# Optimization experiments

Hardware: AMD Instinct MI355X
Metric: run time of the kernel (lower is better)

The kernel has to match this reference:

```python
import jax, jax.numpy as jnp
import numpy as np

B, S, D = 2, 2048, 2048
H, HD = 16, 128          # num_heads, head_dim (H*HD == D)
I = 4096                 # intermediate_size; ffn in-dim is 2*I
EPS = 1e-5


def rmsnorm(x, w):
    return x * jax.lax.rsqrt(jnp.mean(x * x, axis=-1, keepdims=True) + EPS) * w


def setup_inputs() -> dict:
    key = jax.random.key(0)
    ks = jax.random.split(key, 12)
    sd = 0.02
    return {
        "hidden_states": jax.random.normal(ks[0], (B, S, D), jnp.float32),
        "attention_mask": jnp.zeros((B, S), jnp.float32),  # additive mask
        "rn1_w": jnp.ones((D,), jnp.float32),
        "wq": jax.random.normal(ks[1], (D, D), jnp.float32) * sd,
        "wk": jax.random.normal(ks[2], (D, D), jnp.float32) * sd,
        "wv": jax.random.normal(ks[3], (D, D), jnp.float32) * sd,
        "wo": jax.random.normal(ks[4], (D, D), jnp.float32) * sd,
        "rn2_w": jnp.ones((D,), jnp.float32),
        "w1": jax.random.normal(ks[5], (D, 2 * I), jnp.float32) * sd,      # Linear(d, 2*I, bias=False)
        "fc1_w": jax.random.normal(ks[6], (2 * I, I), jnp.float32) * sd,   # SwiGLU fc1
        "fc1_b": jnp.zeros((I,), jnp.float32),
        "fc2_w": jax.random.normal(ks[7], (2 * I, I), jnp.float32) * sd,   # SwiGLU fc2
        "fc2_b": jnp.zeros((I,), jnp.float32),
        "w3": jax.random.normal(ks[8], (I, D), jnp.float32) * sd,          # Linear(I, d, bias=False)
    }


def reference(hidden_states, attention_mask, rn1_w, wq, wk, wv, wo, rn2_w,
              w1, fc1_w, fc1_b, fc2_w, fc2_b, w3):
    # --- attention ---
    attn_in = rmsnorm(hidden_states, rn1_w)
    q = (attn_in @ wq).reshape(B, S, H, HD)
    k = (attn_in @ wk).reshape(B, S, H, HD)
    v = (attn_in @ wv).reshape(B, S, H, HD)
    # rope_cache is None -> no rotary embedding applied
    scores = jnp.einsum("bqhd,bkhd->bhqk", q, k) / np.sqrt(HD).astype(np.float32)
    scores = scores + attention_mask[:, None, None, :]  # [B,1,1,S] broadcast
    probs = jax.nn.softmax(scores, axis=-1)             # dropout p=0 (eval)
    attn = jnp.einsum("bhqk,bkhd->bqhd", probs, v).reshape(B, S, D)
    residual1 = hidden_states + attn @ wo
    # --- SwiGLU FFN ---
    ffn_in = rmsnorm(residual1, rn2_w)
    x = ffn_in @ w1                                      # [B,S,2I]
    gated = jax.nn.silu(x @ fc1_w + fc1_b) * (x @ fc2_w + fc2_b)  # [B,S,I]
    return residual1 + gated @ w3
```

## Files before the change

kernel.cpp:

```cpp
#include <hip/hip_runtime.h>
#include <hip/hip_bf16.h>
#include <stdint.h>

using short8 = __attribute__((ext_vector_type(8))) short;
using uint4v = __attribute__((ext_vector_type(4))) unsigned int;
using f32x4  = __attribute__((ext_vector_type(4))) float;

#define DEV __device__ __forceinline__

DEV float b2f(unsigned short u) {
  union { unsigned int i; float f; } v; v.i = ((unsigned int)u) << 16; return v.f;
}
DEV unsigned short f2b(float f) {
  union { float f; unsigned int i; } v; v.f = f;
  unsigned int x = v.i;
  return (unsigned short)((x + 0x7FFFu + ((x >> 16) & 1u)) >> 16);
}
DEV void g2lds16(const void* g, void* l) {
  __builtin_amdgcn_global_load_lds((const __attribute__((address_space(1))) void*)g,
                                   (__attribute__((address_space(3))) void*)l, 16, 0, 0);
}

DEV void xcd_rect_map(int wg, int nbx, int rby, int rbx, int& by, int& bx) {
  const int xcd_cols = nbx / rbx;
  const int xcd = wg & 7, local = wg >> 3;
  const int xr = xcd / xcd_cols, xc = xcd % xcd_cols;
  by = xr * rby + local / rbx;
  bx = xc * rbx + local % rbx;
}

enum { EPI_BF16 = 0, EPI_RESID_F32 = 1, EPI_BIAS_BF16 = 2, EPI_RESID_OUT = 3, EPI_SWIGLU = 4 };

template<int EPI>
__global__ __launch_bounds__(512, 2)
void gemm_bt256(const unsigned short* __restrict__ A, const unsigned short* __restrict__ Bt,
                void* __restrict__ Cout, const void* __restrict__ extra,
                const void* __restrict__ extra2, int M, int N, int K, int rby, int rbx) {
  __shared__ __align__(16) unsigned short As[2][256 * 64];
  __shared__ __align__(16) unsigned short Bs3[3][256 * 64];
  int by, bx;
  xcd_rect_map(blockIdx.x, N >> 8, rby, rbx, by, bx);
  const int m0 = by << 8, n0 = bx << 8;
  const int t = threadIdx.x;
  const int l = t & 63, wid = t >> 6;
  const int lr = l & 15, lg = l >> 4;
  const int wr = (wid >> 2) << 7;
  const int wc = (wid & 3) << 6;

  f32x4 acc[8][4];
#pragma unroll
  for (int i = 0; i < 8; ++i)
#pragma unroll
    for (int j = 0; j < 4; ++j) acc[i][j] = (f32x4){0.f, 0.f, 0.f, 0.f};

  const int sr = t >> 3;
  const int scSwz = ((t & 7) << 3) ^ ((sr & 7) << 3);
  const unsigned short* Ag = A  + (size_t)(m0 + sr) * K + scSwz;
  const unsigned short* Bg = Bt + (size_t)(n0 + sr) * K + scSwz;
  const int nT = K >> 6;

  const unsigned short* AgNext = Ag + 64;
  const unsigned short* BgNext2 = Bg + 128;
  const size_t rowK64 = (size_t)64 * K;

  const int xorv = (lr & 7) << 3;
  const int cb0 = (lg * 8) ^ xorv;
  const int cb1 = (32 + lg * 8) ^ xorv;

  short8 afA[2][2], afB[2][2], bfrA[4][2], bfrB[4][2];

#define STAGE_A(buf)                                                  \
  {                                                                   \
    unsigned short* dst = &As[buf][t * 8];                            \
    _Pragma("unroll")                                                 \
    for (int ld = 0; ld < 4; ++ld)                                    \
      g2lds16(AgNext + (size_t)ld * rowK64, dst + ld * 4096);         \
  }
#define STAGE_B2(slot)                                                \
  {                                                                   \
    unsigned short* dst = &Bs3[slot][t * 8];                          \
    _Pragma("unroll")                                                 \
    for (int ld = 0; ld < 4; ++ld)                                    \
      g2lds16(BgNext2 + (size_t)ld * rowK64, dst + ld * 4096);        \
  }
#define READ_A(dst, base, p)                                          \
  {                                                                   \
    const int ro0 = (wr + ((p) * 2 + 0) * 16 + lr) << 6;              \
    const int ro1 = (wr + ((p) * 2 + 1) * 16 + lr) << 6;              \
    dst[0][0] = *(const short8*)((base) + ro0 + cb0);                 \
    dst[0][1] = *(const short8*)((base) + ro0 + cb1);                 \
    dst[1][0] = *(const short8*)((base) + ro1 + cb0);                 \
    dst[1][1] = *(const short8*)((base) + ro1 + cb1);                 \
  }
#define READ_B(dst, base)                                             \
  {                                                                   \
    _Pragma("unroll")                                                 \
    for (int ni = 0; ni < 4; ++ni) {                                  \
      const int ro = (wc + ni * 16 + lr) << 6;                        \
      dst[ni][0] = *(const short8*)((base) + ro + cb0);               \
      dst[ni][1] = *(const short8*)((base) + ro + cb1);               \
    }                                                                 \
  }
#define MFMA_PH(af, bfr, r0)                                          \
  {                                                                   \
    _Pragma("unroll")                                                 \
    for (int kk = 0; kk < 2; ++kk)                                    \
      _Pragma("unroll")                                               \
      for (int a = 0; a < 2; ++a)                                     \
        _Pragma("unroll")                                             \
        for (int ni = 0; ni < 4; ++ni)                                \
          acc[(r0) + a][ni] = __builtin_amdgcn_mfma_f32_16x16x32_bf16(\
              af[a][kk], bfr[ni][kk], acc[(r0) + a][ni], 0, 0, 0);    \
  }

#define TILE_BODY(tt, BFR, BFRN)                                      \
  {                                                                   \
    const unsigned short* baseA = &As[(tt) & 1][0];                   \
    const bool more1 = ((tt) + 1) < nT;                               \
    const bool more2 = ((tt) + 2) < nT;                               \
               \
    READ_A(afB, baseA, 1);                                            \
    if (more1) STAGE_A(((tt) + 1) & 1);                               \
    asm volatile("s_waitcnt lgkmcnt(4)" ::: "memory");                \
    __builtin_amdgcn_sched_barrier(0);                                \
    __builtin_amdgcn_s_setprio(1);                                    \
    MFMA_PH(afA, BFR, 0);                                             \
    __builtin_amdgcn_s_setprio(0);                                    \
               \
    READ_A(afA, baseA, 2);                                            \
    if (more2) STAGE_B2(bs2);                                         \
    asm volatile("s_waitcnt lgkmcnt(4)" ::: "memory");                \
    __builtin_amdgcn_sched_barrier(0);                                \
    __builtin_amdgcn_s_setprio(1);                                    \
    MFMA_PH(afB, BFR, 2);                                             \
    __builtin_amdgcn_s_setprio(0);                                    \
       \
    READ_A(afB, baseA, 3);                                            \
    if (more1) {                                                      \
      if (more2) asm volatile("s_waitcnt vmcnt(8)" ::: "memory");     \
      else       asm volatile("s_waitcnt vmcnt(4)" ::: "memory");     \
    }                                                                 \
    asm volatile("s_waitcnt lgkmcnt(4)" ::: "memory");                \
    __builtin_amdgcn_sched_barrier(0);                                \
    __builtin_amdgcn_s_setprio(1);                                    \
    MFMA_PH(afA, BFR, 4);                                             \
    __builtin_amdgcn_s_setprio(0);                                    \
                 \
    if (more1) {                                                      \
      READ_B(BFRN, &Bs3[bnext][0]);                                   \
      asm volatile("s_waitcnt lgkmcnt(8)" ::: "memory");              \
    } else {                                                          \
      asm volatile("s_waitcnt lgkmcnt(0)" ::: "memory");              \
    }                                                                 \
    __builtin_amdgcn_sched_barrier(0);                                \
    __builtin_amdgcn_s_setprio(1);                                    \
    MFMA_PH(afB, BFR, 6);                                             \
    __builtin_amdgcn_s_setprio(0);                                    \
    if (more1) {                                                      \
      if (more2) asm volatile("s_waitcnt vmcnt(4)" ::: "memory");     \
      else       asm volatile("s_waitcnt vmcnt(0)" ::: "memory");     \
      asm volatile("s_barrier" ::: "memory");                         \
      AgNext += 64;                                                   \
      BgNext2 += 64;                                                  \
      bnext = (bnext == 2) ? 0 : bnext + 1;                           \
      bs2  = (bs2 == 2) ? 0 : bs2 + 1;                                \
      READ_A(afA, &As[((tt) + 1) & 1][0], 0);                         \
    }                                                                 \
  }

  {
    unsigned short* dstA = &As[0][t * 8];
    unsigned short* dstB = &Bs3[0][t * 8];
#pragma unroll
    for (int ld = 0; ld < 4; ++ld) {
      g2lds16(Ag + (size_t)ld * rowK64, dstA + ld * 4096);
      g2lds16(Bg + (size_t)ld * rowK64, dstB + ld * 4096);
    }
  }
  {
    unsigned short* dstB1 = &Bs3[1][t * 8];
    const unsigned short* srcB1 = Bg + 64;
#pragma unroll
    for (int ld = 0; ld < 4; ++ld) g2lds16(srcB1 + (size_t)ld * rowK64, dstB1 + ld * 4096);
  }
  asm volatile("s_waitcnt vmcnt(4)\n\ts_barrier" ::: "memory");

  int bnext = 1;
  int bs2 = 2;
  READ_A(afA, &As[0][0], 0);
  READ_B(bfrA, &Bs3[0][0]);

  for (int tp = 0; tp < nT; tp += 2) {
    TILE_BODY(tp,     bfrA, bfrB);
    TILE_BODY(tp + 1, bfrB, bfrA);
  }
#undef STAGE_A
#undef STAGE_B2
#undef READ_A
#undef READ_B
#undef MFMA_PH
#undef TILE_BODY

#pragma unroll
  for (int mi = 0; mi < 8; ++mi) {
#pragma unroll
    for (int ni = 0; ni < 4; ++ni) {
      const int col = n0 + wc + ni * 16 + lr;
#pragma unroll
      for (int j = 0; j < 4; ++j) {
        const int row = m0 + wr + mi * 16 + lg * 4 + j;
        const size_t idx = (size_t)row * N + col;
        const float v = acc[mi][ni][j];
        if constexpr (EPI == EPI_BF16) {
          ((unsigned short*)Cout)[idx] = f2b(v);
        } else if constexpr (EPI == EPI_RESID_F32) {
          ((float*)Cout)[idx] = v + ((const float*)extra)[idx];
        } else if constexpr (EPI == EPI_BIAS_BF16) {
          ((unsigned short*)Cout)[idx] = f2b(v + ((const float*)extra)[col]);
        } else if constexpr (EPI == EPI_SWIGLU) {
          const float g1v = b2f(((const unsigned short*)extra2)[idx]);
          const float v2 = v + ((const float*)extra)[col];
          ((unsigned short*)Cout)[idx] = f2b(g1v / (1.f + __expf(-g1v)) * v2);
        } else {
          ((float*)Cout)[idx] = v + ((const float*)extra)[idx];
        }
      }
    }
  }
}

template<int EPI>
__global__ __launch_bounds__(256)
void gemm_bt(const unsigned short* __restrict__ A, const unsigned short* __restrict__ Bt,
             void* __restrict__ Cout, const void* __restrict__ extra,
             int M, int N, int K, int rby, int rbx) {
  __shared__ __align__(16) unsigned short As[128 * 64];
  __shared__ __align__(16) unsigned short Bs[128 * 64];
  int by, bx;
  xcd_rect_map(blockIdx.x, N >> 7, rby, rbx, by, bx);
  const int m0 = by << 7, n0 = bx << 7;
  const int t = threadIdx.x;
  const int l = t & 63, w = t >> 6;
  const int lr = l & 15, lg = l >> 4;
  const int wr = (w >> 1) << 6, wc = (w & 1) << 6;

  f32x4 acc[4][4];
#pragma unroll
  for (int i = 0; i < 4; ++i)
#pragma unroll
    for (int j = 0; j < 4; ++j) acc[i][j] = (f32x4){0.f, 0.f, 0.f, 0.f};

  const int sr = t >> 3;
  const int skSwz = ((t & 7) << 3) ^ ((sr & 7) << 3);
  const unsigned short* Ag = A  + (size_t)(m0 + sr) * K + skSwz;
  const unsigned short* Bg = Bt + (size_t)(n0 + sr) * K + skSwz;
  unsigned short* Al = As + t * 8;
  unsigned short* Bl = Bs + t * 8;

  for (int kt = 0; kt < K; kt += 64) {
#pragma unroll
    for (int c = 0; c < 4; ++c) {
      g2lds16(Ag + (size_t)(c * 32) * K + kt, Al + c * 2048);
      g2lds16(Bg + (size_t)(c * 32) * K + kt, Bl + c * 2048);
    }
    __syncthreads();
#pragma unroll
    for (int ks = 0; ks < 2; ++ks) {
      short8 af[4], bfr[4];
#pragma unroll
      for (int mi = 0; mi < 4; ++mi) {
        const int row = wr + mi * 16 + lr;
        af[mi] = *(const short8*)(As + (row << 6) + (((ks * 32 + lg * 8)) ^ ((row & 7) << 3)));
      }
#pragma unroll
      for (int ni = 0; ni < 4; ++ni) {
        const int row = wc + ni * 16 + lr;
        bfr[ni] = *(const short8*)(Bs + (row << 6) + (((ks * 32 + lg * 8)) ^ ((row & 7) << 3)));
      }
#pragma unroll
      for (int mi = 0; mi < 4; ++mi)
#pragma unroll
        for (int ni = 0; ni < 4; ++ni)
          acc[mi][ni] = __builtin_amdgcn_mfma_f32_16x16x32_bf16(af[mi], bfr[ni], acc[mi][ni], 0, 0, 0);
    }
    __syncthreads();
  }

#pragma unroll
  for (int mi = 0; mi < 4; ++mi) {
#pragma unroll
    for (int ni = 0; ni < 4; ++ni) {
      const int col = n0 + wc + ni * 16 + lr;
#pragma unroll
      for (int j = 0; j < 4; ++j) {
        const int row = m0 + wr + mi * 16 + lg * 4 + j;
        const size_t idx = (size_t)row * N + col;
        const float v = acc[mi][ni][j];
        if constexpr (EPI == EPI_BF16) {
          ((unsigned short*)Cout)[idx] = f2b(v);
        } else if constexpr (EPI == EPI_RESID_F32) {
          ((float*)Cout)[idx] = v + ((const float*)extra)[idx];
        } else if constexpr (EPI == EPI_BIAS_BF16) {
          ((unsigned short*)Cout)[idx] = f2b(v + ((const float*)extra)[col]);
        } else {
          ((float*)Cout)[idx] = v + ((const float*)extra)[idx];
        }
      }
    }
  }
}

__global__ __launch_bounds__(256)
void attn_fwd(const unsigned short* __restrict__ qkv, const unsigned short* __restrict__ vt,
              const float* __restrict__ mask, unsigned short* __restrict__ out) {
  __shared__ __align__(16) unsigned short Ks[64 * 128];
  __shared__ __align__(16) unsigned short Vs[128 * 64];
  __shared__ __align__(16) unsigned short Ps[4][16 * 64];
  const int b = blockIdx.z, hh = blockIdx.y;
  const int q0 = blockIdx.x << 6;
  const int t = threadIdx.x, l = t & 63, w = t >> 6;
  const int lr = l & 15, lg = l >> 4;
  const float scale = 0.08838834764831845f;

  short8 qf[4];
  {
    const unsigned short* qb = qkv + (size_t)(b * 2048 + q0 + w * 16 + lr) * 6144 + hh * 128;
#pragma unroll
    for (int ks = 0; ks < 4; ++ks) qf[ks] = *(const short8*)(qb + ks * 32 + lg * 8);
  }
  f32x4 acc_o[8];
#pragma unroll
  for (int i = 0; i < 8; ++i) acc_o[i] = (f32x4){0.f, 0.f, 0.f, 0.f};
  float m_r[4], l_r[4];
#pragma unroll
  for (int j = 0; j < 4; ++j) { m_r[j] = -1e30f; l_r[j] = 0.f; }

  const unsigned short* kb = qkv + (size_t)(b * 2048) * 6144 + 2048 + hh * 128;
  const unsigned short* vb = vt + (size_t)(b * 16 + hh) * 128 * 2048;
  const float* mb = mask + b * 2048;

  for (int kt = 0; kt < 2048; kt += 64) {
#pragma unroll
    for (int c = 0; c < 4; ++c) {
      const int e = (c * 256 + t) * 8;
      const int kr = e >> 7, kc = e & 127;
      g2lds16(kb + (size_t)(kt + kr) * 6144 + (kc ^ ((kr & 7) << 3)), Ks + e);
      const int vr = e >> 6, vc = e & 63;
      g2lds16(vb + (size_t)vr * 2048 + kt + (vc ^ ((vr & 7) << 3)), Vs + e);
    }
    __syncthreads();

    f32x4 sc[4];
#pragma unroll
    for (int nt = 0; nt < 4; ++nt) {
      f32x4 s = (f32x4){0.f, 0.f, 0.f, 0.f};
#pragma unroll
      for (int ks = 0; ks < 4; ++ks) {
        short8 kf = *(const short8*)(Ks + ((nt * 16 + lr) << 7) + ((ks * 32 + lg * 8) ^ ((lr & 7) << 3)));
        s = __builtin_amdgcn_mfma_f32_16x16x32_bf16(qf[ks], kf, s, 0, 0, 0);
      }
      sc[nt] = s;
    }
#pragma unroll
    for (int nt = 0; nt < 4; ++nt) {
      const float mv = mb[kt + nt * 16 + lr];
#pragma unroll
      for (int j = 0; j < 4; ++j) sc[nt][j] = sc[nt][j] * scale + mv;
    }
#pragma unroll
    for (int j = 0; j < 4; ++j) {
      float tm = fmaxf(fmaxf(sc[0][j], sc[1][j]), fmaxf(sc[2][j], sc[3][j]));
      tm = fmaxf(tm, __shfl_xor(tm, 1));
      tm = fmaxf(tm, __shfl_xor(tm, 2));
      tm = fmaxf(tm, __shfl_xor(tm, 4));
      tm = fmaxf(tm, __shfl_xor(tm, 8));
      const float mn = fmaxf(m_r[j], tm);
      const float corr = __expf(m_r[j] - mn);
      m_r[j] = mn;
      float ps = 0.f;
#pragma unroll
      for (int nt = 0; nt < 4; ++nt) {
        const float p = __expf(sc[nt][j] - mn);
        sc[nt][j] = p;
        ps += p;
      }
      ps += __shfl_xor(ps, 1);
      ps += __shfl_xor(ps, 2);
      ps += __shfl_xor(ps, 4);
      ps += __shfl_xor(ps, 8);
      l_r[j] = l_r[j] * corr + ps;
#pragma unroll
      for (int di = 0; di < 8; ++di) acc_o[di][j] *= corr;
    }
#pragma unroll
    for (int nt = 0; nt < 4; ++nt)
#pragma unroll
      for (int j = 0; j < 4; ++j) {
        const int q = lg * 4 + j;
        Ps[w][(q << 6) + ((nt * 16 + lr) ^ ((q & 7) << 3))] = f2b(sc[nt][j]);
      }
    asm volatile("s_waitcnt lgkmcnt(0)" ::: "memory");
#pragma unroll
    for (int ks2 = 0; ks2 < 2; ++ks2) {
      short8 pf = *(const short8*)(&Ps[w][(lr << 6) + ((ks2 * 32 + lg * 8) ^ ((lr & 7) << 3))]);
#pragma unroll
      for (int di = 0; di < 8; ++di) {
        short8 vf = *(const short8*)(Vs + ((di * 16 + lr) << 6) + ((ks2 * 32 + lg * 8) ^ ((lr & 7) << 3)));
        acc_o[di] = __builtin_amdgcn_mfma_f32_16x16x32_bf16(pf, vf, acc_o[di], 0, 0, 0);
      }
    }
    __syncthreads();
  }
#pragma unroll
  for (int di = 0; di < 8; ++di)
#pragma unroll
    for (int j = 0; j < 4; ++j) {
      const int q = q0 + w * 16 + lg * 4 + j;
      out[(size_t)(b * 2048 + q) * 2048 + hh * 128 + di * 16 + lr] = f2b(acc_o[di][j] / l_r[j]);
    }
}

__global__ __launch_bounds__(256)
void rmsnorm_k(const float* __restrict__ in, const float* __restrict__ wgt,
               unsigned short* __restrict__ out) {
  __shared__ float red[4];
  const int row = blockIdx.x, t = threadIdx.x;
  const float4* rp = (const float4*)(in + (size_t)row * 2048 + t * 8);
  float4 a = rp[0], b = rp[1];
  float x[8] = {a.x, a.y, a.z, a.w, b.x, b.y, b.z, b.w};
  float s = 0.f;
#pragma unroll
  for (int i = 0; i < 8; ++i) s += x[i] * x[i];
#pragma unroll
  for (int m = 1; m < 64; m <<= 1) s += __shfl_xor(s, m);
  const int l = t & 63, w = t >> 6;
  if (l == 0) red[w] = s;
  __syncthreads();
  const float tot = red[0] + red[1] + red[2] + red[3];
  const float rr = rsqrtf(tot * (1.f / 2048.f) + 1e-5f);
  const float4* wp = (const float4*)(wgt + t * 8);
  float4 wa = wp[0], wb = wp[1];
  float ww[8] = {wa.x, wa.y, wa.z, wa.w, wb.x, wb.y, wb.z, wb.w};
  short8 o;
#pragma unroll
  for (int i = 0; i < 8; ++i) o[i] = (short)f2b(x[i] * rr * ww[i]);
  *(short8*)(out + (size_t)row * 2048 + t * 8) = o;
}

__global__ __launch_bounds__(256)
void transpose2d(const float* __restrict__ in, unsigned short* __restrict__ out,
                 int R, int C) {
  __shared__ __align__(16) unsigned int tile2[64][36];
  const int r0 = blockIdx.y << 6, c0 = blockIdx.x << 6;
  const int t = threadIdx.x;
#pragma unroll
  for (int it = 0; it < 2; ++it) {
    const int p = it * 256 + t;
    const int r2 = p >> 4;
    const int c = (p & 15) << 2;
    const float* src = in + (size_t)(r0 + r2 * 2) * C + c0 + c;
    float4 va = *(const float4*)(src);
    float4 vb = *(const float4*)(src + C);
    tile2[c + 0][r2] = (unsigned int)f2b(va.x) | ((unsigned int)f2b(vb.x) << 16);
    tile2[c + 1][r2] = (unsigned int)f2b(va.y) | ((unsigned int)f2b(vb.y) << 16);
    tile2[c + 2][r2] = (unsigned int)f2b(va.z) | ((unsigned int)f2b(vb.z) << 16);
    tile2[c + 3][r2] = (unsigned int)f2b(va.w) | ((unsigned int)f2b(vb.w) << 16);
  }
  __syncthreads();
#pragma unroll
  for (int it = 0; it < 2; ++it) {
    const int u = it * 256 + t;
    const int rr = u >> 3;
    const int k8 = u & 7;
    uint4v v = *(const uint4v*)(&tile2[rr][k8 * 4]);
    short8 o;
#pragma unroll
    for (int j = 0; j < 4; ++j) {
      o[2 * j]     = (short)(v[j] & 0xFFFFu);
      o[2 * j + 1] = (short)(v[j] >> 16);
    }
    *(short8*)(out + (size_t)(c0 + rr) * R + r0 + k8 * 8) = o;
  }
}

__global__ __launch_bounds__(256)
void transpose_v(const unsigned short* __restrict__ qkv, unsigned short* __restrict__ vt) {
  __shared__ __align__(16) unsigned short tile[64][72];
  const int s0 = blockIdx.x << 6, d0 = blockIdx.y << 6;
  const int z = blockIdx.z;
  const unsigned short* in = qkv + (size_t)((z >> 4) * 2048) * 6144 + 4096 + (z & 15) * 128;
  unsigned short* outp = vt + (size_t)z * 128 * 2048;
  const int t = threadIdx.x;
#pragma unroll
  for (int it = 0; it < 2; ++it) {
    const int e = (it * 256 + t) * 8;
    const int r = e >> 6, cc = e & 63;
    short8 v = *(const short8*)(in + (size_t)(s0 + r) * 6144 + d0 + cc);
#pragma unroll
    for (int i = 0; i < 8; ++i) tile[cc + i][r] = (unsigned short)v[i];
  }
  __syncthreads();
#pragma unroll
  for (int it = 0; it < 2; ++it) {
    const int e = (it * 256 + t) * 8;
    const int rr = e >> 6, kk = e & 63;
    short8 v = *(const short8*)(&tile[rr][kk]);
    *(short8*)(outp + (size_t)(d0 + rr) * 2048 + s0 + kk) = v;
  }
}

extern "C" void kernel_launch(void* const* d_in, const int* in_sizes, int n_in,
                              void* d_out, int out_size, void* d_ws, size_t ws_size,
                              hipStream_t stream) {
  const float* h    = (const float*)d_in[0];
  const float* mask = (const float*)d_in[1];
  const float* rn1w = (const float*)d_in[2];
  const float* wq   = (const float*)d_in[3];
  const float* wk   = (const float*)d_in[4];
  const float* wv   = (const float*)d_in[5];
  const float* wo   = (const float*)d_in[6];
  const float* rn2w = (const float*)d_in[7];
  const float* w1   = (const float*)d_in[8];
  const float* fc1w = (const float*)d_in[9];
  const float* fc1b = (const float*)d_in[10];
  const float* fc2w = (const float*)d_in[11];
  const float* fc2b = (const float*)d_in[12];
  const float* w3   = (const float*)d_in[13];

  char* ws = (char*)d_ws;
  size_t off = 0;
  auto alloc = [&](size_t bytes) { char* p = ws + off; off += (bytes + 255) & ~(size_t)255; return p; };
  unsigned short* bufA = (unsigned short*)alloc(16777216);
  unsigned short* bufB = (unsigned short*)alloc(16777216);
  unsigned short* qkv  = (unsigned short*)alloc(50331648);
  float*          r1f  = (float*)alloc(33554432);
  unsigned short* xbuf = (unsigned short*)alloc(67108864);
  unsigned short* g1   = (unsigned short*)alloc(33554432);
  unsigned short* wt   = (unsigned short*)alloc(67108864);
  if (off > ws_size) return;

  rmsnorm_k<<<4096, 256, 0, stream>>>(h, rn1w, bufA);
  transpose2d<<<dim3(32, 32), 256, 0, stream>>>(wq, wt,                 2048, 2048);
  transpose2d<<<dim3(32, 32), 256, 0, stream>>>(wk, wt + 2048 * 2048,   2048, 2048);
  transpose2d<<<dim3(32, 32), 256, 0, stream>>>(wv, wt + 2 * 2048 * 2048, 2048, 2048);
  gemm_bt256<EPI_BF16><<<384, 512, 0, stream>>>(bufA, wt, qkv, nullptr, nullptr, 4096, 6144, 2048, 8, 6);
  transpose_v<<<dim3(32, 2, 32), 256, 0, stream>>>(qkv, bufB);
  attn_fwd<<<dim3(32, 16, 2), 256, 0, stream>>>(qkv, bufB, mask, bufA);
  transpose2d<<<dim3(32, 32), 256, 0, stream>>>(wo, wt, 2048, 2048);
  gemm_bt<EPI_RESID_F32><<<512, 256, 0, stream>>>(bufA, wt, r1f, h, 4096, 2048, 2048, 8, 8);

  rmsnorm_k<<<4096, 256, 0, stream>>>(r1f, rn2w, bufB);
  transpose2d<<<dim3(128, 32), 256, 0, stream>>>(w1, wt, 2048, 8192);
  gemm_bt256<EPI_BF16><<<512, 512, 0, stream>>>(bufB, wt, xbuf, nullptr, nullptr, 4096, 8192, 2048, 8, 8);
  transpose2d<<<dim3(64, 128), 256, 0, stream>>>(fc1w, wt, 8192, 4096);
  gemm_bt256<EPI_BIAS_BF16><<<256, 512, 0, stream>>>(xbuf, wt, g1, fc1b, nullptr, 4096, 4096, 8192, 4, 8);
  transpose2d<<<dim3(64, 128), 256, 0, stream>>>(fc2w, wt, 8192, 4096);
  unsigned short* gated = qkv;
  gemm_bt256<EPI_SWIGLU><<<256, 512, 0, stream>>>(xbuf, wt, gated, fc2b, g1, 4096, 4096, 8192, 4, 8);
  transpose2d<<<dim3(32, 64), 256, 0, stream>>>(w3, wt, 4096, 2048);
  gemm_bt<EPI_RESID_OUT><<<512, 256, 0, stream>>>(gated, wt, d_out, r1f, 4096, 2048, 4096, 8, 8);
}
```

Baseline: 1.142 ms.

## Double-buffer generic GEMM LDS, add lazy softmax rescale and MFMA priority in attention

The generic gemm_bt kernel gets double-buffered LDS tiles, so the next K-tile's global-to-LDS loads are issued before computing on the current one, with hoisted swizzle offsets and one barrier per tile. The flash-attention kernel skips the running-max update and accumulator rescale whenever the new tile max exceeds the old by at most 8 (wave-uniform check), and raises wave priority around its MFMA blocks. Double buffering doubles gemm_bt's LDS use, which may lower occupancy. The lazy rescale can let exponentials grow up to e^8, which fp32 tolerates, though the probabilities are stored in bf16.

```diff
diff --git a/kernel.cpp b/kernel.cpp
--- a/kernel.cpp
+++ b/kernel.cpp
@@ -118,7 +118,6 @@
     const unsigned short* baseA = &As[(tt) & 1][0];                   \
     const bool more1 = ((tt) + 1) < nT;                               \
     const bool more2 = ((tt) + 2) < nT;                               \
-               \
     READ_A(afB, baseA, 1);                                            \
     if (more1) STAGE_A(((tt) + 1) & 1);                               \
     asm volatile("s_waitcnt lgkmcnt(4)" ::: "memory");                \
@@ -126,7 +125,6 @@
     __builtin_amdgcn_s_setprio(1);                                    \
     MFMA_PH(afA, BFR, 0);                                             \
     __builtin_amdgcn_s_setprio(0);                                    \
-               \
     READ_A(afA, baseA, 2);                                            \
     if (more2) STAGE_B2(bs2);                                         \
     asm volatile("s_waitcnt lgkmcnt(4)" ::: "memory");                \
@@ -134,7 +132,6 @@
     __builtin_amdgcn_s_setprio(1);                                    \
     MFMA_PH(afB, BFR, 2);                                             \
     __builtin_amdgcn_s_setprio(0);                                    \
-       \
     READ_A(afB, baseA, 3);                                            \
     if (more1) {                                                      \
       if (more2) asm volatile("s_waitcnt vmcnt(8)" ::: "memory");     \
@@ -145,7 +142,6 @@
     __builtin_amdgcn_s_setprio(1);                                    \
     MFMA_PH(afA, BFR, 4);                                             \
     __builtin_amdgcn_s_setprio(0);                                    \
-                 \
     if (more1) {                                                      \
       READ_B(BFRN, &Bs3[bnext][0]);                                   \
       asm volatile("s_waitcnt lgkmcnt(8)" ::: "memory");              \
@@ -234,8 +230,8 @@
 void gemm_bt(const unsigned short* __restrict__ A, const unsigned short* __restrict__ Bt,
              void* __restrict__ Cout, const void* __restrict__ extra,
              int M, int N, int K, int rby, int rbx) {
-  __shared__ __align__(16) unsigned short As[128 * 64];
-  __shared__ __align__(16) unsigned short Bs[128 * 64];
+  __shared__ __align__(16) unsigned short As[2][128 * 64];
+  __shared__ __align__(16) unsigned short Bs[2][128 * 64];
   int by, bx;
   xcd_rect_map(blockIdx.x, N >> 7, rby, rbx, by, bx);
   const int m0 = by << 7, n0 = bx << 7;
@@ -254,36 +250,64 @@
   const int skSwz = ((t & 7) << 3) ^ ((sr & 7) << 3);
   const unsigned short* Ag = A  + (size_t)(m0 + sr) * K + skSwz;
   const unsigned short* Bg = Bt + (size_t)(n0 + sr) * K + skSwz;
-  unsigned short* Al = As + t * 8;
-  unsigned short* Bl = Bs + t * 8;
-
-  for (int kt = 0; kt < K; kt += 64) {
+  const int nT = K >> 6;
+
+  const int xorv2 = (lr & 7) << 3;
+  const int c0s = (lg * 8) ^ xorv2;
+  const int c1s = (32 + lg * 8) ^ xorv2;
+
+  {
+    unsigned short* dstA = &As[0][t * 8];
+    unsigned short* dstB = &Bs[0][t * 8];
 #pragma unroll
     for (int c = 0; c < 4; ++c) {
-      g2lds16(Ag + (size_t)(c * 32) * K + kt, Al + c * 2048);
-      g2lds16(Bg + (size_t)(c * 32) * K + kt, Bl + c * 2048);
-    }
-    __syncthreads();
-#pragma unroll
-    for (int ks = 0; ks < 2; ++ks) {
-      short8 af[4], bfr[4];
-#pragma unroll
-      for (int mi = 0; mi < 4; ++mi) {
-        const int row = wr + mi * 16 + lr;
-        af[mi] = *(const short8*)(As + (row << 6) + (((ks * 32 + lg * 8)) ^ ((row & 7) << 3)));
-      }
-#pragma unroll
-      for (int ni = 0; ni < 4; ++ni) {
-        const int row = wc + ni * 16 + lr;
-        bfr[ni] = *(const short8*)(Bs + (row << 6) + (((ks * 32 + lg * 8)) ^ ((row & 7) << 3)));
-      }
+      g2lds16(Ag + (size_t)(c * 32) * K, dstA + c * 2048);
+      g2lds16(Bg + (size_t)(c * 32) * K, dstB + c * 2048);
+    }
+  }
+  asm volatile("s_waitcnt vmcnt(0)\n\ts_barrier" ::: "memory");
+
+  for (int tt = 0; tt < nT; ++tt) {
+    const int cur = tt & 1;
+    const bool more = (tt + 1) < nT;
+    if (more) {
+      unsigned short* dstA = &As[cur ^ 1][t * 8];
+      unsigned short* dstB = &Bs[cur ^ 1][t * 8];
+      const unsigned short* sA = Ag + ((size_t)(tt + 1) << 6);
+      const unsigned short* sB = Bg + ((size_t)(tt + 1) << 6);
+#pragma unroll
+      for (int c = 0; c < 4; ++c) {
+        g2lds16(sA + (size_t)(c * 32) * K, dstA + c * 2048);
+        g2lds16(sB + (size_t)(c * 32) * K, dstB + c * 2048);
+      }
+    }
+    const unsigned short* Ab = &As[cur][0];
+    const unsigned short* Bb = &Bs[cur][0];
+    short8 af[2][4], bfr[2][4];
+#pragma unroll
+    for (int mi = 0; mi < 4; ++mi) {
+      const int ro = (wr + mi * 16 + lr) << 6;
+      af[0][mi] = *(const short8*)(Ab + ro + c0s);
+      af[1][mi] = *(const short8*)(Ab + ro + c1s);
+    }
+#pragma unroll
+    for (int ni = 0; ni < 4; ++ni) {
+      const int ro = (wc + ni * 16 + lr) << 6;
+      bfr[0][ni] = *(const short8*)(Bb + ro + c0s);
+      bfr[1][ni] = *(const short8*)(Bb + ro + c1s);
+    }
+    asm volatile("s_waitcnt lgkmcnt(0)" ::: "memory");
+    __builtin_amdgcn_sched_barrier(0);
+    __builtin_amdgcn_s_setprio(1);
+#pragma unroll
+    for (int ks = 0; ks < 2; ++ks)
 #pragma unroll
       for (int mi = 0; mi < 4; ++mi)
 #pragma unroll
         for (int ni = 0; ni < 4; ++ni)
-          acc[mi][ni] = __builtin_amdgcn_mfma_f32_16x16x32_bf16(af[mi], bfr[ni], acc[mi][ni], 0, 0, 0);
-    }
-    __syncthreads();
+          acc[mi][ni] = __builtin_amdgcn_mfma_f32_16x16x32_bf16(af[ks][mi], bfr[ks][ni], acc[mi][ni], 0, 0, 0);
+    __builtin_amdgcn_s_setprio(0);
+    asm volatile("s_waitcnt vmcnt(0)\n\ts_barrier" ::: "memory");
   }
 
 #pragma unroll
@@ -351,6 +375,7 @@
     __syncthreads();
 
     f32x4 sc[4];
+    __builtin_amdgcn_s_setprio(1);
 #pragma unroll
     for (int nt = 0; nt < 4; ++nt) {
       f32x4 s = (f32x4){0.f, 0.f, 0.f, 0.f};
@@ -361,6 +386,7 @@
       }
       sc[nt] = s;
     }
+    __builtin_amdgcn_s_setprio(0);
 #pragma unroll
     for (int nt = 0; nt < 4; ++nt) {
       const float mv = mb[kt + nt * 16 + lr];
@@ -374,9 +400,14 @@
       tm = fmaxf(tm, __shfl_xor(tm, 2));
       tm = fmaxf(tm, __shfl_xor(tm, 4));
       tm = fmaxf(tm, __shfl_xor(tm, 8));
-      const float mn = fmaxf(m_r[j], tm);
-      const float corr = __expf(m_r[j] - mn);
-      m_r[j] = mn;
+      const bool skip = __all(tm - m_r[j] <= 8.f);
+      float corr = 1.f;
+      float mn = m_r[j];
+      if (!skip) {
+        mn = fmaxf(m_r[j], tm);
+        corr = __expf(m_r[j] - mn);
+        m_r[j] = mn;
+      }
       float ps = 0.f;
 #pragma unroll
       for (int nt = 0; nt < 4; ++nt) {
@@ -389,8 +420,10 @@
       ps += __shfl_xor(ps, 4);
       ps += __shfl_xor(ps, 8);
       l_r[j] = l_r[j] * corr + ps;
-#pragma unroll
-      for (int di = 0; di < 8; ++di) acc_o[di][j] *= corr;
+      if (!skip) {
+#pragma unroll
+        for (int di = 0; di < 8; ++di) acc_o[di][j] *= corr;
+      }
     }
 #pragma unroll
     for (int nt = 0; nt < 4; ++nt)
@@ -400,6 +433,7 @@
         Ps[w][(q << 6) + ((nt * 16 + lr) ^ ((q & 7) << 3))] = f2b(sc[nt][j]);
       }
     asm volatile("s_waitcnt lgkmcnt(0)" ::: "memory");
+    __builtin_amdgcn_s_setprio(1);
 #pragma unroll
     for (int ks2 = 0; ks2 < 2; ++ks2) {
       short8 pf = *(const short8*)(&Ps[w][(lr << 6) + ((ks2 * 32 + lg * 8) ^ ((lr & 7) << 3))]);
@@ -409,6 +443,7 @@
         acc_o[di] = __builtin_amdgcn_mfma_f32_16x16x32_bf16(pf, vf, acc_o[di], 0, 0, 0);
       }
     }
+    __builtin_amdgcn_s_setprio(0);
     __syncthreads();
   }
 #pragma unroll
```

After: 1.152 ms (median of 2 runs). About the same (+0.9%).
